# Performance work log

Measured on AMD Instinct MI355X. Metric: run time of the kernel, lower is better.

The kernel has to match this reference:

```python
import jax, jax.numpy as jnp
import numpy as np

TEMPERATURE = 0.5
NEG_FILL = -1e9


def setup_inputs() -> dict:
    key = jax.random.key(0)
    k1, k2 = jax.random.split(key)
    B, D = 4096, 256
    z1 = jax.random.normal(k1, (B, D), dtype=jnp.float32)
    z2 = jax.random.normal(k2, (B, D), dtype=jnp.float32)
    return {"z1": z1, "z2": z2}


def reference(z1, z2):
    z = jnp.concatenate([z1, z2], axis=0)           # [n, d], n = 2B
    n = z.shape[0]
    half = n // 2
    sim = jnp.matmul(z, z.T) / TEMPERATURE          # [n, n]
    eye = jnp.eye(n, dtype=bool)
    sim = jnp.where(eye, NEG_FILL, sim)
    # targets: positive pair is the other view of the same sample
    idx = jnp.arange(n)
    targets = jnp.where(idx < half, idx + half, idx - half)
    logp = jax.nn.log_softmax(sim, axis=-1)         # stable softmax CE
    loss = -jnp.mean(jnp.take_along_axis(logp, targets[:, None], axis=1))
    return loss
```

## Files before the change

kernel.cpp:

```cpp
#include <hip/hip_runtime.h>

#define NROWS 8192
#define HALF  4096
#define DIM   256
#define JS    16
#define JRANGE 512
#define JTILES 32
#define IPB   256
#define IPW   64

typedef short bf16x8 __attribute__((ext_vector_type(8)));
typedef float f32x4  __attribute__((ext_vector_type(4)));

#define GLOAD16(g, l) __builtin_amdgcn_global_load_lds( \
    (const __attribute__((address_space(1))) unsigned int*)(g), \
    (__attribute__((address_space(3))) unsigned int*)(l), 16, 0, 0)

__device__ __forceinline__ unsigned short f2bf(float f) {
    unsigned int u = __float_as_uint(f);
    u += 0x7FFFu + ((u >> 16) & 1u);
    return (unsigned short)(u >> 16);
}

__global__ void k_prep(const float* __restrict__ z1, const float* __restrict__ z2,
                       unsigned short* __restrict__ zb, float* __restrict__ pos,
                       float* __restrict__ out) {
    if (blockIdx.x == 0 && threadIdx.x == 0) *out = 0.0f;
    const float R2 = 1.41421356237309515f;
    int w = threadIdx.x >> 6, lane = threadIdx.x & 63;
    int row = blockIdx.x * 4 + w;
    float4 a = *(const float4*)(z1 + (size_t)row * DIM + lane * 4);
    float4 b = *(const float4*)(z2 + (size_t)row * DIM + lane * 4);

    uint2 pa, pb;
    pa.x = (unsigned int)f2bf(a.x*R2) | ((unsigned int)f2bf(a.y*R2) << 16);
    pa.y = (unsigned int)f2bf(a.z*R2) | ((unsigned int)f2bf(a.w*R2) << 16);
    pb.x = (unsigned int)f2bf(b.x*R2) | ((unsigned int)f2bf(b.y*R2) << 16);
    pb.y = (unsigned int)f2bf(b.z*R2) | ((unsigned int)f2bf(b.w*R2) << 16);
    *(uint2*)(zb + (size_t)row * DIM + lane * 4)          = pa;
    *(uint2*)(zb + (size_t)(row + HALF) * DIM + lane * 4) = pb;

    float d = a.x * b.x + a.y * b.y + a.z * b.z + a.w * b.w;
    #pragma unroll
    for (int k = 32; k; k >>= 1) d += __shfl_xor(d, k);
    if (lane == 0) pos[row] = 2.0f * d;
}

__global__ __launch_bounds__(256, 2)
void k_main(const unsigned short* __restrict__ zb, float2* __restrict__ part) {
    __shared__ __align__(16) char lds[4][8192];
    char* ldsflat = &lds[0][0];

    const int tid  = threadIdx.x;
    const int w    = tid >> 6;
    const int lane = tid & 63;
    const int col  = lane & 15;
    const int kg   = lane >> 4;
    const int ib   = blockIdx.x & 31;
    const int js   = blockIdx.x >> 5;
    const int iw   = ib * IPB + w * IPW;
    const int jb0  = js * JRANGE;
    const int swz  = (lane & 7) << 4;
    const int dr   = col - kg * 4;

    const char* zbb = (const char*)zb;

    const int jp0 = w * 1024 + lane * 16;
    const int jp1 = 4096 + jp0;
    const int jg0 = jp0 ^ (((jp0 >> 9) & 7) << 4);
    const int jg1 = jp1 ^ (((jp1 >> 9) & 7) << 4);

    bf16x8 bf[4][8];
    {
        int igo[4];
        #pragma unroll
        for (int k = 0; k < 4; ++k) {
            int p = k * 4096 + w * 1024 + lane * 16;
            igo[k] = p ^ (((p >> 9) & 7) << 4);
        }
        #pragma unroll
        for (int p = 0; p < 8; ++p) {
            const char* gib = zbb + (size_t)(ib * IPB + p * 32) * 512;
            #pragma unroll
            for (int k = 0; k < 4; ++k)
                GLOAD16(gib + igo[k], ldsflat + k * 4096 + w * 1024);
            __syncthreads();
            if ((p >> 1) == w) {
                #pragma unroll
                for (int h = 0; h < 2; ++h) {
                    const char* tb = ldsflat + h * 8192;
                    #pragma unroll
                    for (int kk = 0; kk < 8; ++kk)
                        bf[(p & 1) * 2 + h][kk] =
                            *(const bf16x8*)(tb + col * 512 + (((kk << 6) | (kg << 4)) ^ swz));
                }
            }
            __syncthreads();
        }
    }

    float m[4], l[4];
    #pragma unroll
    for (int is = 0; is < 4; ++is) { m[is] = -1e30f; l[is] = 0.0f; }

    const char* ap = ldsflat + col * 512;
    int aoff[8];
    #pragma unroll
    for (int kk = 0; kk < 8; ++kk) aoff[kk] = ((kk << 6) | (kg << 4)) ^ swz;

    const int dt = (iw - jb0) >> 4;
    const char* jbase = zbb + (size_t)jb0 * 512;

#define JSTAGE(T, B) do { \
    GLOAD16(jbase + (size_t)(T) * 8192 + jg0, ldsflat + (B) * 8192 + w * 1024); \
    GLOAD16(jbase + (size_t)(T) * 8192 + jg1, ldsflat + (B) * 8192 + 4096 + w * 1024); \
} while (0)

#define COMPUTE_TILE(B, T) do { \
    bf16x8 af[8]; \
    _Pragma("unroll") \
    for (int kk = 0; kk < 8; ++kk) \
        af[kk] = *(const bf16x8*)(ap + aoff[kk] + (B) * 8192); \
    const int dd = (T) - dt; \
    _Pragma("unroll") \
    for (int is = 0; is < 4; ++is) { \
        f32x4 acc = {0.f, 0.f, 0.f, 0.f}; \
        _Pragma("unroll") \
        for (int kk = 0; kk < 8; ++kk) \
            acc = __builtin_amdgcn_mfma_f32_16x16x32_bf16(af[kk], bf[is][kk], acc, 0, 0, 0); \
        if (dd == is) { \
            _Pragma("unroll") \
            for (int r = 0; r < 4; ++r) if (dr == r) acc[r] = -1e30f; \
        } \
        float t0 = fmaxf(fmaxf(acc[0], acc[1]), fmaxf(acc[2], acc[3])); \
        if (__any(t0 > m[is])) {                  \
            float mn = fmaxf(m[is], t0); \
            l[is] *= __expf(m[is] - mn); \
            m[is] = mn; \
        } \
        l[is] += __expf(acc[0] - m[is]) + __expf(acc[1] - m[is]) \
               + __expf(acc[2] - m[is]) + __expf(acc[3] - m[is]); \
    } \
} while (0)

    JSTAGE(0, 0); JSTAGE(1, 1);
    __syncthreads();

    for (int u = 0; u < 8; ++u) {
        const int t = u * 4;
        JSTAGE(t + 2, 2); JSTAGE(t + 3, 3);
        COMPUTE_TILE(0, t);
        COMPUTE_TILE(1, t + 1);
        __syncthreads();
        if (u < 7) { JSTAGE(t + 4, 0); JSTAGE(t + 5, 1); }
        COMPUTE_TILE(2, t + 2);
        COMPUTE_TILE(3, t + 3);
        __syncthreads();
    }

    #pragma unroll
    for (int is = 0; is < 4; ++is) {
        float mm = m[is], ll = l[is];
        #pragma unroll
        for (int msk = 16; msk <= 32; msk <<= 1) {
            float mo  = __shfl_xor(mm, msk);
            float lo_ = __shfl_xor(ll, msk);
            float mn  = fmaxf(mm, mo);
            ll = ll * __expf(mm - mn) + lo_ * __expf(mo - mn);
            mm = mn;
        }
        if (kg == 0) {
            int i = iw + is * 16 + col;
            part[i * JS + js] = make_float2(mm, ll);
        }
    }
#undef JSTAGE
#undef COMPUTE_TILE
}

__global__ void k_final(const float2* __restrict__ part, const float* __restrict__ pos,
                        float* __restrict__ out) {
    int tid = threadIdx.x;
    int i = blockIdx.x * 256 + tid;
    const float2* p = part + (size_t)i * JS;
    float2 v[JS];
    float M = -3e30f;
    #pragma unroll
    for (int s = 0; s < JS; ++s) { v[s] = p[s]; M = fmaxf(M, v[s].x); }
    float L = 0.0f;
    #pragma unroll
    for (int s = 0; s < JS; ++s) L += v[s].y * __expf(v[s].x - M);
    float loss = M + __logf(L) - pos[i & (HALF - 1)];

    #pragma unroll
    for (int k = 32; k; k >>= 1) loss += __shfl_down(loss, k);
    __shared__ float ps[4];
    int w = tid >> 6, lane = tid & 63;
    if (lane == 0) ps[w] = loss;
    __syncthreads();
    if (tid == 0) atomicAdd(out, (ps[0] + ps[1] + ps[2] + ps[3]) * (1.0f / (float)NROWS));
}

extern "C" void kernel_launch(void* const* d_in, const int* in_sizes, int n_in,
                              void* d_out, int out_size, void* d_ws, size_t ws_size,
                              hipStream_t stream) {
    const float* z1 = (const float*)d_in[0];
    const float* z2 = (const float*)d_in[1];
    float* out = (float*)d_out;

    char* ws = (char*)d_ws;
    unsigned short* zb = (unsigned short*)ws;
    float* pos  = (float*)(ws + 4u * 1024u * 1024u);
    float2* part = (float2*)(ws + 4u * 1024u * 1024u + 65536u);

    k_prep <<<1024, 256, 0, stream>>>(z1, z2, zb, pos, out);
    k_main <<<512,  256, 0, stream>>>(zb, part);
    k_final<<<32,   256, 0, stream>>>(part, pos, out);
}
```

Measured before the change: 101.8 us.

## Fuse final reduction into main kernel via last-block counter; interleave MFMA chains

Removes the separate k_final launch. The last k_main block to finish, found with an atomic ticket counter and thread fences, performs the cross-split log-sum-exp merge and writes the loss directly. Separately, the four MFMA accumulator chains per tile are interleaved so their dependencies overlap, and the online softmax update drops the wave-wide __any branch in favour of an unconditional rescale. The cost is that a single block serially reduces all 8192 rows at the end, and every tile now pays the extra exp for the rescale.

```diff
diff --git a/kernel.cpp b/kernel.cpp
--- a/kernel.cpp
+++ b/kernel.cpp
@@ -24,8 +24,8 @@
 
 __global__ void k_prep(const float* __restrict__ z1, const float* __restrict__ z2,
                        unsigned short* __restrict__ zb, float* __restrict__ pos,
-                       float* __restrict__ out) {
-    if (blockIdx.x == 0 && threadIdx.x == 0) *out = 0.0f;
+                       unsigned* __restrict__ cnt) {
+    if (blockIdx.x == 0 && threadIdx.x == 0) *cnt = 0u;
     const float R2 = 1.41421356237309515f;
     int w = threadIdx.x >> 6, lane = threadIdx.x & 63;
     int row = blockIdx.x * 4 + w;
@@ -47,7 +47,9 @@
 }
 
 __global__ __launch_bounds__(256, 2)
-void k_main(const unsigned short* __restrict__ zb, float2* __restrict__ part) {
+void k_main(const unsigned short* __restrict__ zb, float2* __restrict__ part,
+            const float* __restrict__ pos, unsigned* __restrict__ cnt,
+            float* __restrict__ out) {
     __shared__ __align__(16) char lds[4][8192];
     char* ldsflat = &lds[0][0];
 
@@ -116,31 +118,44 @@
     GLOAD16(jbase + (size_t)(T) * 8192 + jg1, ldsflat + (B) * 8192 + 4096 + w * 1024); \
 } while (0)
 
+#define MASKD(X) do { \
+    _Pragma("unroll") \
+    for (int r = 0; r < 4; ++r) if (dr == r) X[r] = -1e30f; \
+} while (0)
+
+#define LSE_UPD(X, is_) do { \
+    float t0 = fmaxf(fmaxf(X[0], X[1]), fmaxf(X[2], X[3])); \
+    float mn = fmaxf(m[is_], t0); \
+    float rs = __expf(m[is_] - mn); \
+    float e0 = __expf(X[0] - mn), e1 = __expf(X[1] - mn); \
+    float e2 = __expf(X[2] - mn), e3 = __expf(X[3] - mn); \
+    l[is_] = fmaf(l[is_], rs, (e0 + e1) + (e2 + e3)); \
+    m[is_] = mn; \
+} while (0)
+
 #define COMPUTE_TILE(B, T) do { \
     bf16x8 af[8]; \
     _Pragma("unroll") \
     for (int kk = 0; kk < 8; ++kk) \
         af[kk] = *(const bf16x8*)(ap + aoff[kk] + (B) * 8192); \
+    f32x4 a0 = {0.f, 0.f, 0.f, 0.f}; \
+    f32x4 a1 = a0, a2 = a0, a3 = a0; \
+    _Pragma("unroll") \
+    for (int kk = 0; kk < 8; ++kk) { \
+        a0 = __builtin_amdgcn_mfma_f32_16x16x32_bf16(af[kk], bf[0][kk], a0, 0, 0, 0); \
+        a1 = __builtin_amdgcn_mfma_f32_16x16x32_bf16(af[kk], bf[1][kk], a1, 0, 0, 0); \
+        a2 = __builtin_amdgcn_mfma_f32_16x16x32_bf16(af[kk], bf[2][kk], a2, 0, 0, 0); \
+        a3 = __builtin_amdgcn_mfma_f32_16x16x32_bf16(af[kk], bf[3][kk], a3, 0, 0, 0); \
+    } \
     const int dd = (T) - dt; \
-    _Pragma("unroll") \
-    for (int is = 0; is < 4; ++is) { \
-        f32x4 acc = {0.f, 0.f, 0.f, 0.f}; \
-        _Pragma("unroll") \
-        for (int kk = 0; kk < 8; ++kk) \
-            acc = __builtin_amdgcn_mfma_f32_16x16x32_bf16(af[kk], bf[is][kk], acc, 0, 0, 0); \
-        if (dd == is) { \
-            _Pragma("unroll") \
-            for (int r = 0; r < 4; ++r) if (dr == r) acc[r] = -1e30f; \
-        } \
-        float t0 = fmaxf(fmaxf(acc[0], acc[1]), fmaxf(acc[2], acc[3])); \
-        if (__any(t0 > m[is])) {                  \
-            float mn = fmaxf(m[is], t0); \
-            l[is] *= __expf(m[is] - mn); \
-            m[is] = mn; \
-        } \
-        l[is] += __expf(acc[0] - m[is]) + __expf(acc[1] - m[is]) \
-               + __expf(acc[2] - m[is]) + __expf(acc[3] - m[is]); \
-    } \
+    if (dd == 0) MASKD(a0); \
+    if (dd == 1) MASKD(a1); \
+    if (dd == 2) MASKD(a2); \
+    if (dd == 3) MASKD(a3); \
+    LSE_UPD(a0, 0); \
+    LSE_UPD(a1, 1); \
+    LSE_UPD(a2, 2); \
+    LSE_UPD(a3, 3); \
 } while (0)
 
     JSTAGE(0, 0); JSTAGE(1, 1);
@@ -175,30 +190,36 @@
         }
     }
 #undef JSTAGE
+#undef MASKD
+#undef LSE_UPD
 #undef COMPUTE_TILE
-}
-
-__global__ void k_final(const float2* __restrict__ part, const float* __restrict__ pos,
-                        float* __restrict__ out) {
-    int tid = threadIdx.x;
-    int i = blockIdx.x * 256 + tid;
-    const float2* p = part + (size_t)i * JS;
-    float2 v[JS];
-    float M = -3e30f;
-    #pragma unroll
-    for (int s = 0; s < JS; ++s) { v[s] = p[s]; M = fmaxf(M, v[s].x); }
-    float L = 0.0f;
-    #pragma unroll
-    for (int s = 0; s < JS; ++s) L += v[s].y * __expf(v[s].x - M);
-    float loss = M + __logf(L) - pos[i & (HALF - 1)];
-
-    #pragma unroll
-    for (int k = 32; k; k >>= 1) loss += __shfl_down(loss, k);
-    __shared__ float ps[4];
-    int w = tid >> 6, lane = tid & 63;
-    if (lane == 0) ps[w] = loss;
+
+    __threadfence();
+    __shared__ unsigned tok;
+    if (tid == 0) tok = atomicAdd(cnt, 1u);
     __syncthreads();
-    if (tid == 0) atomicAdd(out, (ps[0] + ps[1] + ps[2] + ps[3]) * (1.0f / (float)NROWS));
+    if (tok == (unsigned)(gridDim.x - 1)) {
+        __threadfence();
+        float accl = 0.0f;
+        for (int rr = 0; rr < 32; ++rr) {
+            int i = rr * 256 + tid;
+            const float2* p = part + (size_t)i * JS;
+            float2 v[JS];
+            float M = -3e30f;
+            #pragma unroll
+            for (int s = 0; s < JS; ++s) { v[s] = p[s]; M = fmaxf(M, v[s].x); }
+            float L = 0.0f;
+            #pragma unroll
+            for (int s = 0; s < JS; ++s) L += v[s].y * __expf(v[s].x - M);
+            accl += M + __logf(L) - pos[i & (HALF - 1)];
+        }
+        #pragma unroll
+        for (int k = 32; k; k >>= 1) accl += __shfl_down(accl, k);
+        float* ps = (float*)ldsflat;
+        if ((tid & 63) == 0) ps[tid >> 6] = accl;
+        __syncthreads();
+        if (tid == 0) *out = (ps[0] + ps[1] + ps[2] + ps[3]) * (1.0f / (float)NROWS);
+    }
 }
 
 extern "C" void kernel_launch(void* const* d_in, const int* in_sizes, int n_in,
@@ -210,10 +231,10 @@
 
     char* ws = (char*)d_ws;
     unsigned short* zb = (unsigned short*)ws;
-    float* pos  = (float*)(ws + 4u * 1024u * 1024u);
+    float* pos   = (float*)(ws + 4u * 1024u * 1024u);
+    unsigned* cnt = (unsigned*)(ws + 4u * 1024u * 1024u + 32768u);
     float2* part = (float2*)(ws + 4u * 1024u * 1024u + 65536u);
 
-    k_prep <<<1024, 256, 0, stream>>>(z1, z2, zb, pos, out);
-    k_main <<<512,  256, 0, stream>>>(zb, part);
-    k_final<<<32,   256, 0, stream>>>(part, pos, out);
-}
+    k_prep <<<1024, 256, 0, stream>>>(z1, z2, zb, pos, cnt);
+    k_main <<<512,  256, 0, stream>>>(zb, part, pos, cnt, out);
+}
```

Result: slower. 179.5 us (+76.3%).

## Halve rows per block and double grid to raise occupancy in k_main

Applied to the files above, without the earlier changes.

Each block now owns 128 i-rows (32 per wave) instead of 256, so the register-resident B fragments shrink from 4x8 to 2x8 vectors. The grid doubles to 1024 blocks and launch bounds request 4 blocks per CU. The compute tile interleaves two independent MFMA accumulator chains and splits the A-fragment loads into two halves. The aim is to hide latency through higher occupancy and better MFMA issue. In exchange, every j-tile is streamed from global memory and staged into LDS twice as often per i-row, which doubles that load traffic.

```diff
diff --git a/kernel.cpp b/kernel.cpp
--- a/kernel.cpp
+++ b/kernel.cpp
@@ -6,8 +6,8 @@
 #define JS    16
 #define JRANGE 512
 #define JTILES 32
-#define IPB   256
-#define IPW   64
+#define IPB   128
+#define IPW   32
 
 typedef short bf16x8 __attribute__((ext_vector_type(8)));
 typedef float f32x4  __attribute__((ext_vector_type(4)));
@@ -46,7 +46,7 @@
     if (lane == 0) pos[row] = 2.0f * d;
 }
 
-__global__ __launch_bounds__(256, 2)
+__global__ __launch_bounds__(256, 4)
 void k_main(const unsigned short* __restrict__ zb, float2* __restrict__ part) {
     __shared__ __align__(16) char lds[4][8192];
     char* ldsflat = &lds[0][0];
@@ -56,8 +56,8 @@
     const int lane = tid & 63;
     const int col  = lane & 15;
     const int kg   = lane >> 4;
-    const int ib   = blockIdx.x & 31;
-    const int js   = blockIdx.x >> 5;
+    const int ib   = blockIdx.x & 63;
+    const int js   = blockIdx.x >> 6;
     const int iw   = ib * IPB + w * IPW;
     const int jb0  = js * JRANGE;
     const int swz  = (lane & 7) << 4;
@@ -70,7 +70,7 @@
     const int jg0 = jp0 ^ (((jp0 >> 9) & 7) << 4);
     const int jg1 = jp1 ^ (((jp1 >> 9) & 7) << 4);
 
-    bf16x8 bf[4][8];
+    bf16x8 bf[2][8];
     {
         int igo[4];
         #pragma unroll
@@ -79,19 +79,19 @@
             igo[k] = p ^ (((p >> 9) & 7) << 4);
         }
         #pragma unroll
-        for (int p = 0; p < 8; ++p) {
-            const char* gib = zbb + (size_t)(ib * IPB + p * 32) * 512;
+        for (int q = 0; q < 4; ++q) {
+            const char* gib = zbb + (size_t)(ib * IPB + q * 32) * 512;
             #pragma unroll
             for (int k = 0; k < 4; ++k)
                 GLOAD16(gib + igo[k], ldsflat + k * 4096 + w * 1024);
             __syncthreads();
-            if ((p >> 1) == w) {
+            if (q == w) {
                 #pragma unroll
                 for (int h = 0; h < 2; ++h) {
                     const char* tb = ldsflat + h * 8192;
                     #pragma unroll
                     for (int kk = 0; kk < 8; ++kk)
-                        bf[(p & 1) * 2 + h][kk] =
+                        bf[h][kk] =
                             *(const bf16x8*)(tb + col * 512 + (((kk << 6) | (kg << 4)) ^ swz));
                 }
             }
@@ -99,9 +99,9 @@
         }
     }
 
-    float m[4], l[4];
-    #pragma unroll
-    for (int is = 0; is < 4; ++is) { m[is] = -1e30f; l[is] = 0.0f; }
+    float m[2], l[2];
+    m[0] = m[1] = -1e30f;
+    l[0] = l[1] = 0.0f;
 
     const char* ap = ldsflat + col * 512;
     int aoff[8];
@@ -116,31 +116,47 @@
     GLOAD16(jbase + (size_t)(T) * 8192 + jg1, ldsflat + (B) * 8192 + 4096 + w * 1024); \
 } while (0)
 
+#define MASKD(X) do { \
+    _Pragma("unroll") \
+    for (int r = 0; r < 4; ++r) if (dr == r) X[r] = -1e30f; \
+} while (0)
+
+#define LSE_UPD(X, is_) do { \
+    float t0 = fmaxf(fmaxf(X[0], X[1]), fmaxf(X[2], X[3])); \
+    if (__any(t0 > m[is_])) { \
+        float mn = fmaxf(m[is_], t0); \
+        l[is_] *= __expf(m[is_] - mn); \
+        m[is_] = mn; \
+    } \
+    l[is_] += __expf(X[0] - m[is_]) + __expf(X[1] - m[is_]) \
+            + __expf(X[2] - m[is_]) + __expf(X[3] - m[is_]); \
+} while (0)
+
 #define COMPUTE_TILE(B, T) do { \
-    bf16x8 af[8]; \
-    _Pragma("unroll") \
-    for (int kk = 0; kk < 8; ++kk) \
+    f32x4 a0 = {0.f, 0.f, 0.f, 0.f}; \
+    f32x4 a1 = a0; \
+    bf16x8 af[4]; \
+    _Pragma("unroll") \
+    for (int kk = 0; kk < 4; ++kk) \
         af[kk] = *(const bf16x8*)(ap + aoff[kk] + (B) * 8192); \
+    _Pragma("unroll") \
+    for (int kk = 0; kk < 4; ++kk) { \
+        a0 = __builtin_amdgcn_mfma_f32_16x16x32_bf16(af[kk], bf[0][kk], a0, 0, 0, 0); \
+        a1 = __builtin_amdgcn_mfma_f32_16x16x32_bf16(af[kk], bf[1][kk], a1, 0, 0, 0); \
+    } \
+    _Pragma("unroll") \
+    for (int kk = 0; kk < 4; ++kk) \
+        af[kk] = *(const bf16x8*)(ap + aoff[kk + 4] + (B) * 8192); \
+    _Pragma("unroll") \
+    for (int kk = 0; kk < 4; ++kk) { \
+        a0 = __builtin_amdgcn_mfma_f32_16x16x32_bf16(af[kk], bf[0][kk + 4], a0, 0, 0, 0); \
+        a1 = __builtin_amdgcn_mfma_f32_16x16x32_bf16(af[kk], bf[1][kk + 4], a1, 0, 0, 0); \
+    } \
     const int dd = (T) - dt; \
-    _Pragma("unroll") \
-    for (int is = 0; is < 4; ++is) { \
-        f32x4 acc = {0.f, 0.f, 0.f, 0.f}; \
-        _Pragma("unroll") \
-        for (int kk = 0; kk < 8; ++kk) \
-            acc = __builtin_amdgcn_mfma_f32_16x16x32_bf16(af[kk], bf[is][kk], acc, 0, 0, 0); \
-        if (dd == is) { \
-            _Pragma("unroll") \
-            for (int r = 0; r < 4; ++r) if (dr == r) acc[r] = -1e30f; \
-        } \
-        float t0 = fmaxf(fmaxf(acc[0], acc[1]), fmaxf(acc[2], acc[3])); \
-        if (__any(t0 > m[is])) {                  \
-            float mn = fmaxf(m[is], t0); \
-            l[is] *= __expf(m[is] - mn); \
-            m[is] = mn; \
-        } \
-        l[is] += __expf(acc[0] - m[is]) + __expf(acc[1] - m[is]) \
-               + __expf(acc[2] - m[is]) + __expf(acc[3] - m[is]); \
-    } \
+    if (dd == 0) MASKD(a0); \
+    if (dd == 1) MASKD(a1); \
+    LSE_UPD(a0, 0); \
+    LSE_UPD(a1, 1); \
 } while (0)
 
     JSTAGE(0, 0); JSTAGE(1, 1);
@@ -159,7 +175,7 @@
     }
 
     #pragma unroll
-    for (int is = 0; is < 4; ++is) {
+    for (int is = 0; is < 2; ++is) {
         float mm = m[is], ll = l[is];
         #pragma unroll
         for (int msk = 16; msk <= 32; msk <<= 1) {
@@ -175,6 +191,8 @@
         }
     }
 #undef JSTAGE
+#undef MASKD
+#undef LSE_UPD
 #undef COMPUTE_TILE
 }
 
@@ -214,6 +232,6 @@
     float2* part = (float2*)(ws + 4u * 1024u * 1024u + 65536u);
 
     k_prep <<<1024, 256, 0, stream>>>(z1, z2, zb, pos, out);
-    k_main <<<512,  256, 0, stream>>>(zb, part);
+    k_main <<<1024, 256, 0, stream>>>(zb, part);
     k_final<<<32,   256, 0, stream>>>(part, pos, out);
 }
```

New measurement: 100.6 us. About the same (-1.2%).
